# Optimization experiments

Hardware: AMD Instinct MI355X
Metric: run time of the kernel (lower is better)

Reference implementation:

```python
import math
import jax, jax.numpy as jnp
import numpy as np

HEADS = 8
SCALE_BASE = 512.0
GN_EPS = 1e-5


def _gammas(heads):
    # 1 - exp(linspace(log(1/32), log(1/512), heads))
    return 1.0 - np.exp(np.linspace(math.log(1.0 / 32.0), math.log(1.0 / 512.0), heads))


def _xpos(x, downscale):
    # x: (N, S, d), d even. Faithful to torchscale XPOS with scale_base=512.
    N, S, d = x.shape
    half = d // 2
    scale = (jnp.arange(0, d, 2, dtype=jnp.float32) + 0.4 * d) / (1.4 * d)        # (half,)
    pos = jnp.arange(S, dtype=jnp.float32)
    sc = scale[None, :] ** (pos / SCALE_BASE)[:, None]                             # (S, half)
    inv_freq = 1.0 / (10000.0 ** (jnp.arange(half, dtype=jnp.float32) / half))
    sinusoid = pos[:, None] * inv_freq[None, :]                                    # (S, half)
    sin, cos = jnp.sin(sinusoid), jnp.cos(sinusoid)
    if downscale:
        sc = 1.0 / sc
    # duplicate_interleave == repeat each column twice adjacently
    sin_s = jnp.repeat(sin * sc, 2, axis=-1)                                       # (S, d)
    cos_s = jnp.repeat(cos * sc, 2, axis=-1)
    x1, x2 = x[..., ::2], x[..., 1::2]
    rot = jnp.stack((-x2, x1), axis=-1).reshape(x.shape)                           # rotate_every_two
    return x * cos_s + rot * sin_s


def setup_inputs() -> dict:
    key = jax.random.key(0)
    ks = jax.random.split(key, 6)
    B, S, H = 2, 2048, 1024
    h = HEADS
    d = H // h
    X = jax.random.normal(ks[0], (B, S, H), dtype=jnp.float32)
    # per-head projections, torch init: randn(d, d) / d
    W_Q = jax.random.normal(ks[1], (h, d, d), dtype=jnp.float32) / d
    W_K = jax.random.normal(ks[2], (h, d, d), dtype=jnp.float32) / d
    W_V = jax.random.normal(ks[3], (h, d, d), dtype=jnp.float32) / d
    W_G = jax.random.normal(ks[4], (H, H), dtype=jnp.float32) / H
    W_O = jax.random.normal(ks[5], (H, H), dtype=jnp.float32) / H
    gn_weight = jnp.ones((H,), dtype=jnp.float32)
    gn_bias = jnp.zeros((H,), dtype=jnp.float32)
    return {"X": X, "W_Q": W_Q, "W_K": W_K, "W_V": W_V,
            "W_G": W_G, "W_O": W_O, "gn_weight": gn_weight, "gn_bias": gn_bias}


def reference(X, W_Q, W_K, W_V, W_G, W_O, gn_weight, gn_bias):
    B, S, H = X.shape
    h = HEADS
    d = H // h
    gammas = jnp.asarray(_gammas(h), dtype=X.dtype)                                # (h,)

    Xh = X.reshape(B, S, h, d)
    Q = jnp.einsum('bshd,hde->bhse', Xh, W_Q)                                      # (B,h,S,d)
    K = jnp.einsum('bshd,hde->bhse', Xh, W_K)
    V = jnp.einsum('bshd,hde->bhse', Xh, W_V)

    Q = _xpos(Q.reshape(B * h, S, d), downscale=False).reshape(B, h, S, d)
    K = _xpos(K.reshape(B * h, S, d), downscale=True).reshape(B, h, S, d)

    # decay mask D[h, n, m] = gamma_h^(n-m) for n >= m else 0 (NaN-safe)
    n = jnp.arange(S)
    diff = n[:, None] - n[None, :]                                                 # (S,S)
    causal = (diff >= 0)
    D = (gammas[:, None, None] ** jnp.where(causal, diff, 0).astype(X.dtype)) \
        * causal[None].astype(X.dtype)                                             # (h,S,S)

    att = jnp.einsum('bhsd,bhtd->bhst', Q, K) * D[None]                            # (B,h,S,S)
    Y = jnp.einsum('bhst,bhtd->bshd', att, V).reshape(B, S, H)

    # GroupNorm(heads, hidden) over flattened (B*S, H), biased variance
    Yg = Y.reshape(B * S, h, d)
    mu = Yg.mean(axis=-1, keepdims=True)
    var = Yg.var(axis=-1, keepdims=True)
    Yn = ((Yg - mu) / jnp.sqrt(var + GN_EPS)).reshape(B * S, H)
    Yn = (Yn * gn_weight + gn_bias).reshape(B, S, H)

    G = X @ W_G
    return (G * jax.nn.sigmoid(G) * Yn) @ W_O
```

## Files before the change

### kernel.cpp

```cpp
#include <hip/hip_runtime.h>
#include <math.h>

#define NB 2
#define SEQ 2048
#define HD 1024
#define NH 8
#define DH 128
#define HALF 64

typedef __bf16 bf16_t;
typedef __attribute__((ext_vector_type(8))) __bf16 bf16x8;
typedef __attribute__((ext_vector_type(4))) __bf16 bf16x4;
typedef __attribute__((ext_vector_type(4))) float f32x4;

typedef __attribute__((address_space(1))) void gvoid;
typedef __attribute__((address_space(3))) void lvoid;

__device__ __forceinline__ void gld16(const bf16_t* g, bf16_t* l) {
  __builtin_amdgcn_global_load_lds((gvoid*)g, (lvoid*)l, 16, 0, 0);
}

__device__ __forceinline__ float head_l2g(int hh) {
  double ga = log(1.0/32.0), gbb = log(1.0/512.0);
  float gamma = (float)(1.0 - exp(ga + (double)hh * (gbb - ga) / 7.0));
  return log2f(gamma);
}

__device__ void wsplit_body(const float* __restrict__ in, bf16_t* __restrict__ oh,
                            int M, int N, int bx, int by, int z,
                            float (*tile)[65]) {
  in += (size_t)z * M * N; oh += (size_t)z * M * N;
  int r0 = by * 64, c0 = bx * 64;
  int t = threadIdx.x;
  for (int idx = t; idx < 1024; idx += 256) {
    int r = idx >> 4, c4 = (idx & 15) * 4;
    float4 v = *(const float4*)(in + (size_t)(r0 + r) * N + c0 + c4);
    *(float4*)&tile[r][c4] = v;
  }
  __syncthreads();
  for (int idx = t; idx < 1024; idx += 256) {
    int c = idx >> 4, r4 = (idx & 15) * 4;
    bf16x4 h;
    #pragma unroll
    for (int j = 0; j < 4; ++j)
      h[j] = (bf16_t)tile[r4 + j][c];
    *(bf16x4*)(oh + (size_t)(c0 + c) * M + r0 + r4) = h;
  }
}

__global__ __launch_bounds__(256) void k_prep(
    const float* __restrict__ Wq, const float* __restrict__ Wk,
    const float* __restrict__ Wv, const float* __restrict__ Wg,
    const float* __restrict__ Wo,
    float* __restrict__ tabs, bf16_t* __restrict__ Wqt,
    bf16_t* __restrict__ Wkt, bf16_t* __restrict__ Wvt,
    bf16_t* __restrict__ Wgt, bf16_t* __restrict__ Wot) {
  __shared__ float tile[64][65];
  int b = blockIdx.x;
  if (b < 512) {
    int idx = b * 256 + threadIdx.x;
    int s = idx >> 6, i = idx & 63;
    float dd = (float)DH;
    float scale = (2.0f * (float)i + 0.4f * dd) / (1.4f * dd);
    float sc = expf(logf(scale) * ((float)s / 512.0f));
    float inv_freq = expf(-logf(10000.0f) * ((float)i / (float)HALF));
    float ang = (float)s * inv_freq;
    float sn, cs;
    sincosf(ang, &sn, &cs);
    float rsc = 1.0f / sc;
    tabs[idx]               = sn * sc;
    tabs[SEQ*HALF + idx]    = cs * sc;
    tabs[2*SEQ*HALF + idx]  = sn * rsc;
    tabs[3*SEQ*HALF + idx]  = cs * rsc;
  } else if (b < 608) {
    int i = b - 512;
    int which = i >> 5;
    int j = i & 31;
    const float* in = (which == 0) ? Wq : (which == 1) ? Wk : Wv;
    bf16_t* oh = (which == 0) ? Wqt : (which == 1) ? Wkt : Wvt;
    wsplit_body(in, oh, DH, DH, j & 1, (j >> 1) & 1, j >> 2, tile);
  } else {
    int i = b - 608;
    int which = i >> 8;
    int j = i & 255;
    wsplit_body(which ? Wo : Wg, which ? Wot : Wgt, HD, HD,
                j & 15, j >> 4, 0, tile);
  }
}

__global__ __launch_bounds__(256, 2) void k_qkv(
    const float* __restrict__ X, const float* __restrict__ tabs,
    const bf16_t* __restrict__ Wqt, const bf16_t* __restrict__ Wkt,
    const bf16_t* __restrict__ Wvt,
    bf16_t* __restrict__ Qo, bf16_t* __restrict__ Ko,
    bf16_t* __restrict__ VTo, bf16_t* __restrict__ Xhg) {
  __shared__ bf16_t Wsh[128][128];
  int t = threadIdx.x;
  int lane = t & 63, w = t >> 6;
  int lr = lane & 15, lg = lane >> 4;
  int s0 = blockIdx.x * 64;
  int hh = blockIdx.y;
  int b  = blockIdx.z;
  size_t bh = (size_t)(b*NH + hh);

  bf16x8 xh[4];
  {
    const float* xp = X + ((size_t)(b*SEQ + s0 + 16*w + lr)) * HD + hh*DH + 8*lg;
    #pragma unroll
    for (int ks = 0; ks < 4; ++ks) {
      float4 u = *(const float4*)(xp + 32*ks);
      float4 v = *(const float4*)(xp + 32*ks + 4);
      float fv[8] = {u.x,u.y,u.z,u.w,v.x,v.y,v.z,v.w};
      #pragma unroll
      for (int j = 0; j < 8; ++j) xh[ks][j] = (bf16_t)fv[j];
    }
  }
  {
    bf16_t* xo = Xhg + ((size_t)(b*SEQ + s0 + 16*w + lr)) * HD + hh*DH + 8*lg;
    #pragma unroll
    for (int ks = 0; ks < 4; ++ks)
      *(bf16x8*)(xo + 32*ks) = xh[ks];
  }

  const bf16_t* Wp[3] = {Wqt, Wkt, Wvt};

  for (int which = 0; which < 3; ++which) {
    const bf16_t* wp = Wp[which] + (size_t)hh * (DH*DH);
    __syncthreads();
    for (int idx = t; idx < 2048; idx += 256) {
      int e = idx >> 4, kb = idx & 15;
      int kbs = kb ^ (e & 7);
      *(bf16x8*)&Wsh[e][kbs*8] = *(const bf16x8*)(wp + (size_t)e*DH + kb*8);
    }
    __syncthreads();
    f32x4 yacc[8];
    #pragma unroll
    for (int i = 0; i < 8; ++i) yacc[i] = (f32x4){0.f,0.f,0.f,0.f};
    #pragma unroll
    for (int sub = 0; sub < 8; ++sub) {
      int e = 16*sub + lr;
      #pragma unroll
      for (int ks = 0; ks < 4; ++ks) {
        int ch = (lg + 4*ks) ^ (lr & 7);
        bf16x8 bhv = *(const bf16x8*)&Wsh[e][ch*8];
        yacc[sub] = __builtin_amdgcn_mfma_f32_16x16x32_bf16(xh[ks], bhv, yacc[sub], 0, 0, 0);
      }
    }
    if (which < 2) {
      const float* st = tabs + (which ? 2*SEQ*HALF : 0);
      const float* ct = st + SEQ*HALF;
      bf16_t* Op = which ? Ko : Qo;
      #pragma unroll
      for (int sub = 0; sub < 8; ++sub) {
        int e = 16*sub + lr;
        int i = e >> 1;
        #pragma unroll
        for (int reg = 0; reg < 4; ++reg) {
          float v = yacc[sub][reg];
          float p = __shfl_xor(v, 1);
          int srow = s0 + 16*w + 4*lg + reg;
          float sv = st[srow*HALF + i], cv = ct[srow*HALF + i];
          float o = v * cv + ((e & 1) ? p : -p) * sv;
          Op[(bh*SEQ + srow) * DH + e] = (bf16_t)o;
        }
      }
    } else {
      #pragma unroll
      for (int sub = 0; sub < 8; ++sub) {
        int e = 16*sub + lr;
        bf16x4 hv;
        #pragma unroll
        for (int reg = 0; reg < 4; ++reg)
          hv[reg] = (bf16_t)yacc[sub][reg];
        *(bf16x4*)(VTo + bh * (size_t)(DH*SEQ) + (size_t)e*SEQ + (s0 + 16*w + 4*lg)) = hv;
      }
    }
  }
}

__global__ __launch_bounds__(256, 1) void k_delta(
    const bf16_t* __restrict__ Kg, const bf16_t* __restrict__ VTg,
    bf16_t* __restrict__ DSt) {
  __shared__ bf16_t KT[128][128];
  __shared__ bf16_t Vd[128][128];
  int t = threadIdx.x;
  int lane = t & 63, w = t >> 6;
  int lr = lane & 15, lg = lane >> 4;
  int c = blockIdx.x, bh = blockIdx.y, hh = bh & 7;
  float l2g = head_l2g(hh);
  size_t kbase = (size_t)bh * SEQ * DH + (size_t)c * 128 * DH;
  size_t vtb   = (size_t)bh * DH * SEQ + (size_t)c * 128;

  for (int idx = t; idx < 2048; idx += 256) {
    int dc = idx >> 7, tau = idx & 127;
    bf16x8 h8 = *(const bf16x8*)(Kg + kbase + (size_t)tau*DH + dc*8);
    #pragma unroll
    for (int j = 0; j < 8; ++j) {
      int d = dc*8 + j;
      int col = (((tau>>3) ^ (d & 7)) << 3) | (tau & 7);
      KT[d][col] = h8[j];
    }
  }
  for (int idx = t; idx < 2048; idx += 256) {
    int dv = idx >> 4, tc = idx & 15;
    bf16x8 h8 = *(const bf16x8*)(VTg + vtb + (size_t)dv*SEQ + tc*8);
    bf16x8 oh;
    #pragma unroll
    for (int j = 0; j < 8; ++j) {
      int tau = tc*8 + j;
      oh[j] = (bf16_t)((float)h8[j] * exp2f(l2g * (float)(127 - tau)));
    }
    int cs = tc ^ (dv & 7);
    *(bf16x8*)&Vd[dv][cs*8] = oh;
  }
  __syncthreads();

  f32x4 acc[2][8];
  #pragma unroll
  for (int i = 0; i < 2; ++i)
    #pragma unroll
    for (int s = 0; s < 8; ++s) acc[i][s] = (f32x4){0.f,0.f,0.f,0.f};

  #pragma unroll
  for (int i = 0; i < 2; ++i) {
    int dv = 32*w + 16*i + lr;
    #pragma unroll
    for (int ks = 0; ks < 4; ++ks) {
      int ca = (lg + 4*ks) ^ (dv & 7);
      bf16x8 avh = *(const bf16x8*)&Vd[dv][ca*8];
      #pragma unroll
      for (int sub = 0; sub < 8; ++sub) {
        int dk = 16*sub + lr;
        int cb = (lg + 4*ks) ^ (dk & 7);
        bf16x8 bkh = *(const bf16x8*)&KT[dk][cb*8];
        acc[i][sub] = __builtin_amdgcn_mfma_f32_16x16x32_bf16(avh, bkh, acc[i][sub], 0, 0, 0);
      }
    }
  }
  size_t obase = ((size_t)bh * 16 + c) * 16384;
  #pragma unroll
  for (int i = 0; i < 2; ++i)
    #pragma unroll
    for (int sub = 0; sub < 8; ++sub)
      #pragma unroll
      for (int reg = 0; reg < 4; ++reg) {
        int dv = 32*w + 16*i + 4*lg + reg;
        int dk = 16*sub + lr;
        DSt[obase + (size_t)dv*128 + dk] = (bf16_t)acc[i][sub][reg];
      }
}

__global__ __launch_bounds__(256) void k_scan(bf16_t* __restrict__ DSt) {
  int t = threadIdx.x;
  int bh = blockIdx.y, hh = bh & 7;
  float l2g = head_l2g(hh);
  float g128 = exp2f(l2g * 128.0f);
  int dv = blockIdx.x * 16 + (t >> 4);
  int dk0 = (t & 15) * 8;
  size_t base = ((size_t)bh * 16) * 16384 + (size_t)dv*128 + dk0;
  float S[8] = {};
  for (int c = 0; c < 16; ++c) {
    size_t off = base + (size_t)c * 16384;
    bf16x8 dh = *(const bf16x8*)(DSt + off);
    bf16x8 sh;
    #pragma unroll
    for (int j = 0; j < 8; ++j) sh[j] = (bf16_t)S[j];
    *(bf16x8*)(DSt + off) = sh;
    #pragma unroll
    for (int j = 0; j < 8; ++j)
      S[j] = g128*S[j] + (float)dh[j];
  }
}

__global__ __launch_bounds__(512, 1) void k_ret(
    const bf16_t* __restrict__ Qg, const bf16_t* __restrict__ Kg,
    const bf16_t* __restrict__ VTg, const bf16_t* __restrict__ DSt,
    const float* __restrict__ gw, const float* __restrict__ gb,
    bf16_t* __restrict__ Yn) {
  __shared__ bf16_t Ksh[64][128];
  __shared__ bf16_t Vsh[128][64];
  __shared__ bf16_t Ph[128][64];
  int t = threadIdx.x;
  int lane = t & 63, w = t >> 6;
  int lr = lane & 15, lg = lane >> 4;
  int c = blockIdx.x, bh = blockIdx.y, hh = bh & 7;
  int s0 = c * 128;
  size_t base  = (size_t)bh * SEQ * DH;
  size_t vbase = (size_t)bh * DH * SEQ;
  float l2g = head_l2g(hh);
  float colf = exp2f(-l2g * (float)lr);
  float g16v[4];
  #pragma unroll
  for (int ts = 0; ts < 4; ++ts) g16v[ts] = exp2f(-l2g * (float)(16*ts));

  bf16x8 qh[4];
  {
    const bf16_t* qp = Qg + base + (size_t)(s0 + 16*w + lr) * DH + lg * 8;
    #pragma unroll
    for (int ks = 0; ks < 4; ++ks)
      qh[ks] = *(const bf16x8*)(qp + 32*ks);
  }
  f32x4 yacc[8];
  #pragma unroll
  for (int i = 0; i < 8; ++i) yacc[i] = (f32x4){0.f,0.f,0.f,0.f};

  for (int idx = t; idx < 1024; idx += 512) {
    int r = idx >> 4, kb = idx & 15;
    int kbs = kb ^ (r & 7);
    *(bf16x8*)&Ksh[r][kbs*8] = *(const bf16x8*)(Kg + base + (size_t)(s0 + r)*DH + kb*8);
  }
  for (int idx = t; idx < 1024; idx += 512) {
    int d = idx >> 3, cb = idx & 7;
    int cbs = cb ^ (d & 7);
    *(bf16x8*)&Vsh[d][cbs*8] = *(const bf16x8*)(VTg + vbase + (size_t)d*SEQ + s0 + cb*8);
  }

  {
    const bf16_t* sth = DSt + ((size_t)bh * 16 + c) * 16384;
    #pragma unroll
    for (int sub = 0; sub < 8; ++sub) {
      size_t ro = (size_t)(16*sub + lr) * 128 + 8*lg;
      #pragma unroll
      for (int ks = 0; ks < 4; ++ks) {
        bf16x8 bh_ = *(const bf16x8*)(sth + ro + 32*ks);
        yacc[sub] = __builtin_amdgcn_mfma_f32_16x16x32_bf16(qh[ks], bh_, yacc[sub], 0, 0, 0);
      }
    }
    float rowc[4];
    #pragma unroll
    for (int reg = 0; reg < 4; ++reg)
      rowc[reg] = exp2f(l2g * (float)(16*w + 4*lg + reg + 1));
    #pragma unroll
    for (int sub = 0; sub < 8; ++sub)
      #pragma unroll
      for (int reg = 0; reg < 4; ++reg)
        yacc[sub][reg] *= rowc[reg];
  }
  __syncthreads();

  for (int kt = 0; kt < 2; ++kt) {
    int t0 = kt * 64;
    if (kt == 1) {
      __syncthreads();
      for (int idx = t; idx < 1024; idx += 512) {
        int r = idx >> 4, kb = idx & 15;
        int kbs = kb ^ (r & 7);
        *(bf16x8*)&Ksh[r][kbs*8] = *(const bf16x8*)(Kg + base + (size_t)(s0 + 64 + r)*DH + kb*8);
      }
      for (int idx = t; idx < 1024; idx += 512) {
        int d = idx >> 3, cb = idx & 7;
        int cbs = cb ^ (d & 7);
        *(bf16x8*)&Vsh[d][cbs*8] = *(const bf16x8*)(VTg + vbase + (size_t)d*SEQ + s0 + 64 + cb*8);
      }
    }
    __syncthreads();
    if (!(kt == 1 && w < 4)) {
      float rowf[4];
      #pragma unroll
      for (int reg = 0; reg < 4; ++reg)
        rowf[reg] = exp2f(l2g * (float)(16*w + 4*lg + reg - t0));

      #pragma unroll
      for (int ts = 0; ts < 4; ++ts) {
        f32x4 sacc = (f32x4){0.f,0.f,0.f,0.f};
        int trow = 16*ts + lr;
        #pragma unroll
        for (int ks = 0; ks < 4; ++ks) {
          int kbs = (4*ks + lg) ^ (trow & 7);
          bf16x8 kh8 = *(const bf16x8*)&Ksh[trow][kbs*8];
          sacc = __builtin_amdgcn_mfma_f32_16x16x32_bf16(qh[ks], kh8, sacc, 0, 0, 0);
        }
        float cf = colf * g16v[ts];
        #pragma unroll
        for (int reg = 0; reg < 4; ++reg) {
          int qloc = 4*lg + reg;
          int diff = (16*w + qloc) - (t0 + trow);
          float p = (diff >= 0) ? sacc[reg] * (rowf[reg] * cf) : 0.0f;
          int cb = (trow >> 3) ^ (qloc & 7);
          Ph[16*w + qloc][cb*8 + (trow & 7)] = (bf16_t)p;
        }
      }
      #pragma unroll
      for (int ks = 0; ks < 2; ++ks) {
        int prow = 16*w + lr;
        int pcb = (4*ks + lg) ^ (lr & 7);
        bf16x8 pah = *(const bf16x8*)&Ph[prow][pcb*8];
        #pragma unroll
        for (int sub = 0; sub < 8; ++sub) {
          int drow = 16*sub + lr;
          int vcb = (4*ks + lg) ^ (drow & 7);
          bf16x8 vh8 = *(const bf16x8*)&Vsh[drow][vcb*8];
          yacc[sub] = __builtin_amdgcn_mfma_f32_16x16x32_bf16(pah, vh8, yacc[sub], 0, 0, 0);
        }
      }
    }
  }

  float s1v[4] = {0.f,0.f,0.f,0.f}, s2v[4] = {0.f,0.f,0.f,0.f};
  #pragma unroll
  for (int sub = 0; sub < 8; ++sub)
    #pragma unroll
    for (int reg = 0; reg < 4; ++reg) {
      float v = yacc[sub][reg];
      s1v[reg] += v;
      s2v[reg] += v * v;
    }
  #pragma unroll
  for (int off = 8; off; off >>= 1)
    #pragma unroll
    for (int reg = 0; reg < 4; ++reg) {
      s1v[reg] += __shfl_xor(s1v[reg], off);
      s2v[reg] += __shfl_xor(s2v[reg], off);
    }
  float gwv[8], gbv[8];
  #pragma unroll
  for (int sub = 0; sub < 8; ++sub) {
    gwv[sub] = gw[hh*DH + 16*sub + lr];
    gbv[sub] = gb[hh*DH + 16*sub + lr];
  }
  int b = bh >> 3;
  #pragma unroll
  for (int reg = 0; reg < 4; ++reg) {
    float mean = s1v[reg] * (1.0f/128.0f);
    float var = s2v[reg] * (1.0f/128.0f) - mean*mean;
    float inv = rsqrtf(var + 1e-5f);
    int srow = s0 + 16*w + 4*lg + reg;
    bf16_t* op = Yn + (size_t)(b*SEQ + srow) * HD + hh*DH;
    #pragma unroll
    for (int sub = 0; sub < 8; ++sub)
      op[16*sub + lr] = (bf16_t)((yacc[sub][reg] - mean) * inv * gwv[sub] + gbv[sub]);
  }
}

__global__ __launch_bounds__(256, 2) void k_gemm(
    const bf16_t* __restrict__ Ag, const bf16_t* __restrict__ Bg,
    const bf16_t* __restrict__ E,
    bf16_t* __restrict__ Oh, float* __restrict__ Of, int mode) {
  __shared__ bf16_t SA[2][64][64];
  __shared__ bf16_t SBB[2][128][64];
  int t = threadIdx.x;
  int lane = t & 63, w = t >> 6;
  int lr = lane & 15, lg = lane >> 4;
  int wr = w >> 1, wc = w & 1;
  int bid = blockIdx.x;
  int xcd = bid & 7, local = bid >> 3;
  int mp = xcd * 8 + (local >> 3);
  int np = local & 7;
  int m0 = mp * 64, n0 = np * 128;

  const bf16_t* As = Ag + (size_t)m0 * HD;
  const bf16_t* Bs = Bg + (size_t)n0 * HD;

  f32x4 acc[2][4];
  #pragma unroll
  for (int i = 0; i < 2; ++i)
    #pragma unroll
    for (int j = 0; j < 4; ++j) acc[i][j] = (f32x4){0.f,0.f,0.f,0.f};

  int srow = lane >> 3, sch = lane & 7;

  {
    #pragma unroll
    for (int i = 0; i < 2; ++i) {
      int row = w*16 + i*8 + srow;
      int kc = (sch ^ (row & 7)) * 8;
      gld16(As + (size_t)row*HD + kc, &SA[0][w*16 + i*8][0]);
    }
    #pragma unroll
    for (int i = 0; i < 4; ++i) {
      int row = w*32 + i*8 + srow;
      int kc = (sch ^ (row & 7)) * 8;
      gld16(Bs + (size_t)row*HD + kc, &SBB[0][w*32 + i*8][0]);
    }
  }
  __syncthreads();

  int buf = 0;
  for (int kt = 0; kt < 16; ++kt) {
    if (kt + 1 < 16) {
      int k0 = (kt + 1) * 64;
      #pragma unroll
      for (int i = 0; i < 2; ++i) {
        int row = w*16 + i*8 + srow;
        int kc = (sch ^ (row & 7)) * 8;
        gld16(As + (size_t)row*HD + k0 + kc, &SA[buf^1][w*16 + i*8][0]);
      }
      #pragma unroll
      for (int i = 0; i < 4; ++i) {
        int row = w*32 + i*8 + srow;
        int kc = (sch ^ (row & 7)) * 8;
        gld16(Bs + (size_t)row*HD + k0 + kc, &SBB[buf^1][w*32 + i*8][0]);
      }
    }
    #pragma unroll
    for (int ks = 0; ks < 2; ++ks) {
      bf16x8 a_[2], b_[4];
      #pragma unroll
      for (int mf = 0; mf < 2; ++mf) {
        int row = wr*32 + mf*16 + lr;
        int ch = (lg + 4*ks) ^ (row & 7);
        a_[mf] = *(const bf16x8*)&SA[buf][row][ch*8];
      }
      #pragma unroll
      for (int nf = 0; nf < 4; ++nf) {
        int row = wc*64 + nf*16 + lr;
        int ch = (lg + 4*ks) ^ (row & 7);
        b_[nf] = *(const bf16x8*)&SBB[buf][row][ch*8];
      }
      #pragma unroll
      for (int mf = 0; mf < 2; ++mf)
        #pragma unroll
        for (int nf = 0; nf < 4; ++nf)
          acc[mf][nf] = __builtin_amdgcn_mfma_f32_16x16x32_bf16(a_[mf], b_[nf], acc[mf][nf], 0, 0, 0);
    }
    __syncthreads();
    buf ^= 1;
  }
  #pragma unroll
  for (int mf = 0; mf < 2; ++mf) {
    #pragma unroll
    for (int nf = 0; nf < 4; ++nf) {
      #pragma unroll
      for (int reg = 0; reg < 4; ++reg) {
        int m = m0 + wr*32 + mf*16 + 4*lg + reg;
        int n = n0 + wc*64 + nf*16 + lr;
        float g = acc[mf][nf][reg];
        size_t off = (size_t)m * HD + n;
        if (mode == 1) {
          float sg = 1.0f / (1.0f + expf(-g));
          Oh[off] = (bf16_t)(g * sg * (float)E[off]);
        } else {
          Of[off] = g;
        }
      }
    }
  }
}

extern "C" void kernel_launch(void* const* d_in, const int* in_sizes, int n_in,
                              void* d_out, int out_size, void* d_ws, size_t ws_size,
                              hipStream_t stream) {
  const float* X  = (const float*)d_in[0];
  const float* Wq = (const float*)d_in[1];
  const float* Wk = (const float*)d_in[2];
  const float* Wv = (const float*)d_in[3];
  const float* Wg = (const float*)d_in[4];
  const float* Wo = (const float*)d_in[5];
  const float* gw = (const float*)d_in[6];
  const float* gb = (const float*)d_in[7];
  float* out = (float*)d_out;
  float* ws = (float*)d_ws;

  float* tabs = ws;
  bf16_t* Q   = (bf16_t*)(ws + 524288);
  bf16_t* K   = Q + 4194304;
  bf16_t* VT  = K + 4194304;
  bf16_t* Yn  = VT + 4194304;
  bf16_t* DSt = Yn + 4194304;
  bf16_t* Wqt = DSt + 4194304;
  bf16_t* Wkt = Wqt + 131072;
  bf16_t* Wvt = Wkt + 131072;
  bf16_t* Wgt = Wvt + 131072;
  bf16_t* Wot = Wgt + 1048576;
  bf16_t* Xh  = Wot + 1048576;
  bf16_t* A2  = Q;

  k_prep<<<dim3(1120), dim3(256), 0, stream>>>(Wq, Wk, Wv, Wg, Wo, tabs,
                                               Wqt, Wkt, Wvt, Wgt, Wot);
  k_qkv<<<dim3(32, 8, 2), dim3(256), 0, stream>>>(X, tabs, Wqt, Wkt, Wvt,
                                                  Q, K, VT, Xh);
  k_delta<<<dim3(16, 16), dim3(256), 0, stream>>>(K, VT, DSt);
  k_scan<<<dim3(8, 16), dim3(256), 0, stream>>>(DSt);
  k_ret<<<dim3(16, 16), dim3(512), 0, stream>>>(Q, K, VT, DSt, gw, gb, Yn);
  k_gemm<<<dim3(512), dim3(256), 0, stream>>>(Xh, Wgt, Yn, A2, nullptr, 1);
  k_gemm<<<dim3(512), dim3(256), 0, stream>>>(A2, Wot, nullptr, nullptr, out, 0);
}
```

Before: 108.0 us.

## Fuse QKV projection with per-chunk delta state computation

Merges the QKV projection kernel and the chunk delta-state kernel into one. Each 512-thread block now handles a 128-token chunk, writing K and decayed V straight into shared memory and running the V^T K product there, so K and V are no longer re-read from global memory. This removes one kernel launch and that global round trip. In exchange the grid shrinks to 256 blocks with one block per CU and higher shared-memory use, which may lower occupancy.

```diff
diff --git a/kernel.cpp b/kernel.cpp
--- a/kernel.cpp
+++ b/kernel.cpp
@@ -88,20 +88,23 @@
   }
 }
 
-__global__ __launch_bounds__(256, 2) void k_qkv(
+__global__ __launch_bounds__(512, 1) void k_qkvd(
     const float* __restrict__ X, const float* __restrict__ tabs,
     const bf16_t* __restrict__ Wqt, const bf16_t* __restrict__ Wkt,
     const bf16_t* __restrict__ Wvt,
     bf16_t* __restrict__ Qo, bf16_t* __restrict__ Ko,
-    bf16_t* __restrict__ VTo, bf16_t* __restrict__ Xhg) {
+    bf16_t* __restrict__ VTo, bf16_t* __restrict__ Xhg,
+    bf16_t* __restrict__ DSt) {
   __shared__ bf16_t Wsh[128][128];
+  __shared__ bf16_t KT[128][128];
+  __shared__ bf16_t Vd[128][128];
   int t = threadIdx.x;
   int lane = t & 63, w = t >> 6;
   int lr = lane & 15, lg = lane >> 4;
-  int s0 = blockIdx.x * 64;
-  int hh = blockIdx.y;
-  int b  = blockIdx.z;
+  int c = blockIdx.x, hh = blockIdx.y, b = blockIdx.z;
+  int s0 = c * 128;
   size_t bh = (size_t)(b*NH + hh);
+  float l2g = head_l2g(hh);
 
   bf16x8 xh[4];
   {
@@ -127,7 +130,7 @@
   for (int which = 0; which < 3; ++which) {
     const bf16_t* wp = Wp[which] + (size_t)hh * (DH*DH);
     __syncthreads();
-    for (int idx = t; idx < 2048; idx += 256) {
+    for (int idx = t; idx < 2048; idx += 512) {
       int e = idx >> 4, kb = idx & 15;
       int kbs = kb ^ (e & 7);
       *(bf16x8*)&Wsh[e][kbs*8] = *(const bf16x8*)(wp + (size_t)e*DH + kb*8);
@@ -158,72 +161,46 @@
         for (int reg = 0; reg < 4; ++reg) {
           float v = yacc[sub][reg];
           float p = __shfl_xor(v, 1);
-          int srow = s0 + 16*w + 4*lg + reg;
+          int tau = 16*w + 4*lg + reg;
+          int srow = s0 + tau;
           float sv = st[srow*HALF + i], cv = ct[srow*HALF + i];
           float o = v * cv + ((e & 1) ? p : -p) * sv;
-          Op[(bh*SEQ + srow) * DH + e] = (bf16_t)o;
+          bf16_t ob = (bf16_t)o;
+          Op[(bh*SEQ + srow) * DH + e] = ob;
+          if (which == 1) {
+            int col = (((tau>>3) ^ (e & 7)) << 3) | (tau & 7);
+            KT[e][col] = ob;
+          }
         }
       }
     } else {
+      float decay[4];
+      #pragma unroll
+      for (int reg = 0; reg < 4; ++reg)
+        decay[reg] = exp2f(l2g * (float)(127 - (16*w + 4*lg + reg)));
       #pragma unroll
       for (int sub = 0; sub < 8; ++sub) {
         int e = 16*sub + lr;
         bf16x4 hv;
         #pragma unroll
-        for (int reg = 0; reg < 4; ++reg)
-          hv[reg] = (bf16_t)yacc[sub][reg];
+        for (int reg = 0; reg < 4; ++reg) {
+          int tau = 16*w + 4*lg + reg;
+          float f = yacc[sub][reg];
+          hv[reg] = (bf16_t)f;
+          int col = (((tau>>3) ^ (e & 7)) << 3) | (tau & 7);
+          Vd[e][col] = (bf16_t)(f * decay[reg]);
+        }
         *(bf16x4*)(VTo + bh * (size_t)(DH*SEQ) + (size_t)e*SEQ + (s0 + 16*w + 4*lg)) = hv;
       }
     }
   }
-}
-
-__global__ __launch_bounds__(256, 1) void k_delta(
-    const bf16_t* __restrict__ Kg, const bf16_t* __restrict__ VTg,
-    bf16_t* __restrict__ DSt) {
-  __shared__ bf16_t KT[128][128];
-  __shared__ bf16_t Vd[128][128];
-  int t = threadIdx.x;
-  int lane = t & 63, w = t >> 6;
-  int lr = lane & 15, lg = lane >> 4;
-  int c = blockIdx.x, bh = blockIdx.y, hh = bh & 7;
-  float l2g = head_l2g(hh);
-  size_t kbase = (size_t)bh * SEQ * DH + (size_t)c * 128 * DH;
-  size_t vtb   = (size_t)bh * DH * SEQ + (size_t)c * 128;
-
-  for (int idx = t; idx < 2048; idx += 256) {
-    int dc = idx >> 7, tau = idx & 127;
-    bf16x8 h8 = *(const bf16x8*)(Kg + kbase + (size_t)tau*DH + dc*8);
-    #pragma unroll
-    for (int j = 0; j < 8; ++j) {
-      int d = dc*8 + j;
-      int col = (((tau>>3) ^ (d & 7)) << 3) | (tau & 7);
-      KT[d][col] = h8[j];
-    }
-  }
-  for (int idx = t; idx < 2048; idx += 256) {
-    int dv = idx >> 4, tc = idx & 15;
-    bf16x8 h8 = *(const bf16x8*)(VTg + vtb + (size_t)dv*SEQ + tc*8);
-    bf16x8 oh;
-    #pragma unroll
-    for (int j = 0; j < 8; ++j) {
-      int tau = tc*8 + j;
-      oh[j] = (bf16_t)((float)h8[j] * exp2f(l2g * (float)(127 - tau)));
-    }
-    int cs = tc ^ (dv & 7);
-    *(bf16x8*)&Vd[dv][cs*8] = oh;
-  }
   __syncthreads();
 
-  f32x4 acc[2][8];
-  #pragma unroll
-  for (int i = 0; i < 2; ++i)
-    #pragma unroll
-    for (int s = 0; s < 8; ++s) acc[i][s] = (f32x4){0.f,0.f,0.f,0.f};
-
-  #pragma unroll
-  for (int i = 0; i < 2; ++i) {
-    int dv = 32*w + 16*i + lr;
+  f32x4 acc[8];
+  #pragma unroll
+  for (int s = 0; s < 8; ++s) acc[s] = (f32x4){0.f,0.f,0.f,0.f};
+  {
+    int dv = 16*w + lr;
     #pragma unroll
     for (int ks = 0; ks < 4; ++ks) {
       int ca = (lg + 4*ks) ^ (dv & 7);
@@ -233,21 +210,19 @@
         int dk = 16*sub + lr;
         int cb = (lg + 4*ks) ^ (dk & 7);
         bf16x8 bkh = *(const bf16x8*)&KT[dk][cb*8];
-        acc[i][sub] = __builtin_amdgcn_mfma_f32_16x16x32_bf16(avh, bkh, acc[i][sub], 0, 0, 0);
-      }
-    }
-  }
-  size_t obase = ((size_t)bh * 16 + c) * 16384;
-  #pragma unroll
-  for (int i = 0; i < 2; ++i)
-    #pragma unroll
-    for (int sub = 0; sub < 8; ++sub)
-      #pragma unroll
-      for (int reg = 0; reg < 4; ++reg) {
-        int dv = 32*w + 16*i + 4*lg + reg;
-        int dk = 16*sub + lr;
-        DSt[obase + (size_t)dv*128 + dk] = (bf16_t)acc[i][sub][reg];
-      }
+        acc[sub] = __builtin_amdgcn_mfma_f32_16x16x32_bf16(avh, bkh, acc[sub], 0, 0, 0);
+      }
+    }
+  }
+  size_t obase = (bh * 16 + c) * 16384;
+  #pragma unroll
+  for (int sub = 0; sub < 8; ++sub)
+    #pragma unroll
+    for (int reg = 0; reg < 4; ++reg) {
+      int dv = 16*w + 4*lg + reg;
+      int dk = 16*sub + lr;
+      DSt[obase + (size_t)dv*128 + dk] = (bf16_t)acc[sub][reg];
+    }
 }
 
 __global__ __launch_bounds__(256) void k_scan(bf16_t* __restrict__ DSt) {
@@ -567,9 +542,8 @@
 
   k_prep<<<dim3(1120), dim3(256), 0, stream>>>(Wq, Wk, Wv, Wg, Wo, tabs,
                                                Wqt, Wkt, Wvt, Wgt, Wot);
-  k_qkv<<<dim3(32, 8, 2), dim3(256), 0, stream>>>(X, tabs, Wqt, Wkt, Wvt,
-                                                  Q, K, VT, Xh);
-  k_delta<<<dim3(16, 16), dim3(256), 0, stream>>>(K, VT, DSt);
+  k_qkvd<<<dim3(16, 8, 2), dim3(512), 0, stream>>>(X, tabs, Wqt, Wkt, Wvt,
+                                                   Q, K, VT, Xh, DSt);
   k_scan<<<dim3(8, 16), dim3(256), 0, stream>>>(DSt);
   k_ret<<<dim3(16, 16), dim3(512), 0, stream>>>(Q, K, VT, DSt, gw, gb, Yn);
   k_gemm<<<dim3(512), dim3(256), 0, stream>>>(Xh, Wgt, Yn, A2, nullptr, 1);
```

Result: faster. 98.10 us (-9.2%).
